# Kernel optimization log

Hardware: AMD Instinct MI355X
Metric: run time of the kernel (lower is better)

The kernel has to match this reference:

```python
import jax, jax.numpy as jnp
import numpy as np

DIM = 512
HEADS = 8
DIM_HEAD = 64
INNER = HEADS * DIM_HEAD  # 512
EPS = 1e-5
SCALE = DIM_HEAD ** (-0.5)


def setup_inputs() -> dict:
    key = jax.random.key(0)
    ks = jax.random.split(key, 12)
    B, S = 8, 1024
    x = jax.random.normal(ks[0], (B, DIM, S, 1), dtype=jnp.float32)
    # BatchNorm2d params (eval mode: running stats)
    bn_gamma = jax.random.normal(ks[1], (DIM,), dtype=jnp.float32) * 0.1 + 1.0
    bn_beta = jax.random.normal(ks[2], (DIM,), dtype=jnp.float32) * 0.1
    bn_mean = jax.random.normal(ks[3], (DIM,), dtype=jnp.float32) * 0.1
    bn_var = jax.random.uniform(ks[4], (DIM,), dtype=jnp.float32, minval=0.5, maxval=1.5)
    # 1x1 Conv2d == linear: weight [out, in], bias [out]
    def lin(k, out_d, in_d):
        kw, kb = jax.random.split(k)
        lim = 1.0 / np.sqrt(in_d)
        w = jax.random.uniform(kw, (out_d, in_d), dtype=jnp.float32, minval=-lim, maxval=lim)
        b = jax.random.uniform(kb, (out_d,), dtype=jnp.float32, minval=-lim, maxval=lim)
        return w, b
    wq, bq = lin(ks[5], INNER, DIM)
    wk, bk = lin(ks[6], INNER, DIM)
    wv, bv = lin(ks[7], INNER, DIM)
    wo, bo = lin(ks[8], DIM, INNER)
    return {"x": x, "bn_gamma": bn_gamma, "bn_beta": bn_beta,
            "bn_mean": bn_mean, "bn_var": bn_var,
            "wq": wq, "bq": bq, "wk": wk, "bk": bk,
            "wv": wv, "bv": bv, "wo": wo, "bo": bo}


def reference(x, bn_gamma, bn_beta, bn_mean, bn_var,
              wq, bq, wk, bk, wv, bv, wo, bo):
    B, C, S, _ = x.shape
    # BatchNorm2d (eval) over channel dim
    inv = jax.lax.rsqrt(bn_var + EPS)
    xn = (x - bn_mean[None, :, None, None]) * (bn_gamma * inv)[None, :, None, None] \
         + bn_beta[None, :, None, None]
    t = jnp.transpose(xn[..., 0], (0, 2, 1))  # [B, S, C]
    q = (t @ wq.T + bq).reshape(B, S, HEADS, DIM_HEAD)
    k = (t @ wk.T + bk).reshape(B, S, HEADS, DIM_HEAD)
    v = (t @ wv.T + bv).reshape(B, S, HEADS, DIM_HEAD)
    scores = jnp.einsum('bshd,bthd->bhst', q, k) * SCALE  # [B,H,S,S]
    attn = jax.nn.softmax(scores, axis=-1)
    o = jnp.einsum('bhst,bthd->bshd', attn, v).reshape(B, S, INNER)
    y = o @ wo.T + bo  # [B, S, C]
    return jnp.transpose(y, (0, 2, 1))[..., None]  # [B, C, S, 1]
```

## Files before the change

kernel.cpp:

```cpp
#include <hip/hip_runtime.h>
#include <stdint.h>

typedef __bf16 bf16;
typedef bf16 bf16x8 __attribute__((ext_vector_type(8)));
typedef bf16 bf16x4 __attribute__((ext_vector_type(4)));
typedef float f32x4 __attribute__((ext_vector_type(4)));

#define NB 8
#define NS 1024
#define NC 512
#define NH 8
#define ND 64

#define QSCALE 0.18033688011f

__device__ __forceinline__ void gload16(const void* g, void* l) {
  __builtin_amdgcn_global_load_lds(
      (const __attribute__((address_space(1))) void*)g,
      (__attribute__((address_space(3))) void*)l, 16, 0, 0);
}

__global__ __launch_bounds__(256) void bn_tr_kernel(
    const float* __restrict__ x, const float* __restrict__ gam,
    const float* __restrict__ bet, const float* __restrict__ mu,
    const float* __restrict__ var, bf16* __restrict__ t) {
  __shared__ float tile[32][33];
  const int b = blockIdx.z, c0 = blockIdx.y * 32, s0 = blockIdx.x * 32;
  const int tx = threadIdx.x, sj = tx & 31, ci = tx >> 5;
#pragma unroll
  for (int kk = 0; kk < 4; ++kk) {
    const int c = c0 + ci + (kk << 3);
    const float sc = gam[c] * rsqrtf(var[c] + 1e-5f);
    const float sh = bet[c] - mu[c] * sc;
    tile[ci + (kk << 3)][sj] = x[(size_t)(b * NC + c) * NS + s0 + sj] * sc + sh;
  }
  __syncthreads();
#pragma unroll
  for (int kk = 0; kk < 4; ++kk) {
    const int s = s0 + ci + (kk << 3);
    t[(size_t)(b * NS + s) * NC + c0 + sj] = (bf16)tile[sj][ci + (kk << 3)];
  }
}

__global__ __launch_bounds__(256) void wconv_kernel(
    const float* __restrict__ wq, const float* __restrict__ wk,
    const float* __restrict__ wv, const float* __restrict__ wo,
    bf16* __restrict__ wqb, bf16* __restrict__ wkb, bf16* __restrict__ wvb,
    bf16* __restrict__ wob) {
  const int i = (blockIdx.x * 256 + threadIdx.x) * 4;
  float4 a = *(const float4*)(&wq[i]);
  float4 b = *(const float4*)(&wk[i]);
  float4 c = *(const float4*)(&wv[i]);
  float4 d = *(const float4*)(&wo[i]);
  bf16x4 av = {(bf16)a.x, (bf16)a.y, (bf16)a.z, (bf16)a.w};
  bf16x4 bv = {(bf16)b.x, (bf16)b.y, (bf16)b.z, (bf16)b.w};
  bf16x4 cv = {(bf16)c.x, (bf16)c.y, (bf16)c.z, (bf16)c.w};
  bf16x4 dv = {(bf16)d.x, (bf16)d.y, (bf16)d.z, (bf16)d.w};
  *(bf16x4*)(&wqb[i]) = av;
  *(bf16x4*)(&wkb[i]) = bv;
  *(bf16x4*)(&wvb[i]) = cv;
  *(bf16x4*)(&wob[i]) = dv;
}

__global__ __launch_bounds__(256) void gemm_qkv_kernel(
    const bf16* __restrict__ t, const bf16* __restrict__ wqb,
    const bf16* __restrict__ wkb, const bf16* __restrict__ wvb,
    const float* __restrict__ bq, const float* __restrict__ bk,
    const float* __restrict__ bv, bf16* __restrict__ qo, bf16* __restrict__ ko,
    bf16* __restrict__ vo) {
  __shared__ __align__(16) bf16 As[128 * 32];
  __shared__ __align__(16) bf16 Bs[128 * 32];
  const int tid = threadIdx.x;
  const int m0 = blockIdx.x * 128, n0 = blockIdx.y * 128;
  const int wsel = n0 >> 9;
  const bf16* W = (wsel == 0) ? wqb : (wsel == 1 ? wkb : wvb);
  const float* bias = (wsel == 0) ? bq : (wsel == 1 ? bk : bv);
  const int nb = n0 & 511;
  const int w = tid >> 6, lane = tid & 63, l15 = lane & 15, l4 = lane >> 4;
  const int wm = (w >> 1) << 6, wn = (w & 1) << 6;

  const int srl = lane >> 2, sp = lane & 3;
  const int r0 = w * 16 + srl, r1 = 64 + w * 16 + srl;
  const int c0off = (sp ^ ((r0 >> 1) & 3)) << 3;
  const int c1off = (sp ^ ((r1 >> 1) & 3)) << 3;
  const bf16* a0 = t + (size_t)(m0 + r0) * 512 + c0off;
  const bf16* a1 = t + (size_t)(m0 + r1) * 512 + c1off;
  const bf16* b0 = W + (size_t)(nb + r0) * 512 + c0off;
  const bf16* b1 = W + (size_t)(nb + r1) * 512 + c1off;

  f32x4 acc[4][4] = {};
  for (int k0 = 0; k0 < 512; k0 += 32) {
    __syncthreads();
    gload16(a0 + k0, &As[w * 512]);
    gload16(a1 + k0, &As[2048 + w * 512]);
    gload16(b0 + k0, &Bs[w * 512]);
    gload16(b1 + k0, &Bs[2048 + w * 512]);
    __syncthreads();
    bf16x8 af[4], bfv[4];
#pragma unroll
    for (int mi = 0; mi < 4; ++mi) {
      const int row = wm + mi * 16 + l15;
      af[mi] = *(const bf16x8*)(&As[row * 32 + ((l4 ^ ((row >> 1) & 3)) << 3)]);
    }
#pragma unroll
    for (int ni = 0; ni < 4; ++ni) {
      const int row = wn + ni * 16 + l15;
      bfv[ni] = *(const bf16x8*)(&Bs[row * 32 + ((l4 ^ ((row >> 1) & 3)) << 3)]);
    }
#pragma unroll
    for (int mi = 0; mi < 4; ++mi)
#pragma unroll
      for (int ni = 0; ni < 4; ++ni)
        acc[mi][ni] = __builtin_amdgcn_mfma_f32_16x16x32_bf16(af[mi], bfv[ni],
                                                              acc[mi][ni], 0, 0, 0);
  }
  const int bidx = m0 >> 10;
  const int sbase = (m0 & 1023) + wm + (l4 << 2);
  if (wsel == 2) {
#pragma unroll
    for (int ni = 0; ni < 4; ++ni) {
      const int nn = nb + wn + ni * 16 + l15;
      const int hh = nn >> 6, dd = nn & 63;
      const float bsv = bias[nn];
      bf16* vbase = vo + (size_t)(bidx * NH + hh) * (ND * NS) + (size_t)dd * NS + sbase;
#pragma unroll
      for (int mi = 0; mi < 4; ++mi) {
        bf16x4 pk;
#pragma unroll
        for (int r = 0; r < 4; ++r) pk[r] = (bf16)(acc[mi][ni][r] + bsv);
        *(bf16x4*)(&vbase[mi * 16]) = pk;
      }
    }
  } else {
    const bool isq = (wsel == 0);
    bf16* outp = isq ? qo : ko;
#pragma unroll
    for (int ni = 0; ni < 4; ++ni) {
      const int nn = nb + wn + ni * 16 + l15;
      const int hh = nn >> 6, dd = nn & 63;
      const float bsv = bias[nn];
      bf16* obase = outp + (size_t)(bidx * NH + hh) * (NS * ND) + dd;
#pragma unroll
      for (int mi = 0; mi < 4; ++mi) {
#pragma unroll
        for (int r = 0; r < 4; ++r) {
          float val = acc[mi][ni][r] + bsv;
          if (isq) val *= QSCALE;
          obase[(size_t)(sbase + mi * 16 + r) * ND] = (bf16)val;
        }
      }
    }
  }
}

__global__ __launch_bounds__(512) void attn_kernel(const bf16* __restrict__ qg,
                                                   const bf16* __restrict__ kg,
                                                   const bf16* __restrict__ vtg,
                                                   bf16* __restrict__ og) {
  __shared__ __align__(16) bf16 Kb[2][64 * 64];
  __shared__ __align__(16) bf16 Vb[2][64 * 64];
  __shared__ __align__(16) bf16 Ps[8][16 * 64];
  const int bh = blockIdx.y, q0 = blockIdx.x * 128;
  const int tid = threadIdx.x, w = tid >> 6, lane = tid & 63;
  const int l15 = lane & 15, l4 = lane >> 4;
  const bf16* Qp = qg + ((size_t)bh * NS + q0) * ND;
  const bf16* Kp = kg + (size_t)bh * NS * ND;
  const bf16* Vp = vtg + (size_t)bh * ND * NS;

  bf16x8 qf[2];
#pragma unroll
  for (int kk = 0; kk < 2; ++kk)
    qf[kk] = *(const bf16x8*)(&Qp[(size_t)(w * 16 + l15) * ND + ((kk << 2) + l4) * 8]);

  const int srow = w * 8 + (lane >> 3);
  const int soff = ((lane & 7) ^ (srow & 7)) << 3;
  const bf16* ksrc = Kp + (size_t)srow * ND + soff;
  const bf16* vsrc = Vp + (size_t)srow * NS + soff;

  int foff[4][2];
#pragma unroll
  for (int rt = 0; rt < 4; ++rt) {
    const int row = rt * 16 + l15;
    foff[rt][0] = row * 64 + ((l4 ^ (row & 7)) << 3);
    foff[rt][1] = row * 64 + (((4 + l4) ^ (row & 7)) << 3);
  }

  f32x4 oacc[4] = {};
  float mrun = -1e30f, lrun = 0.f;

  gload16(ksrc, &Kb[0][w * 512]);
  gload16(vsrc, &Vb[0][w * 512]);
  __syncthreads();

  int buf = 0;
  for (int kv0 = 0; kv0 < NS; kv0 += 64, buf ^= 1) {
    if (kv0 + 64 < NS) {
      gload16(ksrc + (size_t)(kv0 + 64) * ND, &Kb[buf ^ 1][w * 512]);
      gload16(vsrc + (kv0 + 64), &Vb[buf ^ 1][w * 512]);
    }
    const bf16* Ks = Kb[buf];
    const bf16* Vs = Vb[buf];
    f32x4 st[4];
#pragma unroll
    for (int rt = 0; rt < 4; ++rt) {
      const bf16x8 a0 = *(const bf16x8*)(&Ks[foff[rt][0]]);
      const bf16x8 a1 = *(const bf16x8*)(&Ks[foff[rt][1]]);
      f32x4 z = {0.f, 0.f, 0.f, 0.f};
      z = __builtin_amdgcn_mfma_f32_16x16x32_bf16(a0, qf[0], z, 0, 0, 0);
      st[rt] = __builtin_amdgcn_mfma_f32_16x16x32_bf16(a1, qf[1], z, 0, 0, 0);
    }
    float pm = -1e30f;
#pragma unroll
    for (int rt = 0; rt < 4; ++rt)
#pragma unroll
      for (int r = 0; r < 4; ++r) pm = fmaxf(pm, st[rt][r]);
    pm = fmaxf(pm, __shfl_xor(pm, 16));
    pm = fmaxf(pm, __shfl_xor(pm, 32));
    if (!__all(pm - mrun <= 8.f)) {
      const float mnew = fmaxf(mrun, pm);
      const float alpha = __builtin_amdgcn_exp2f(mrun - mnew);
      float av[4];
#pragma unroll
      for (int r = 0; r < 4; ++r) av[r] = __shfl(alpha, (l4 << 2) + r);
#pragma unroll
      for (int di = 0; di < 4; ++di)
#pragma unroll
        for (int r = 0; r < 4; ++r) oacc[di][r] *= av[r];
      lrun *= alpha;
      mrun = mnew;
    }
    float rs = 0.f;
#pragma unroll
    for (int rt = 0; rt < 4; ++rt) {
      bf16x4 pk;
#pragma unroll
      for (int r = 0; r < 4; ++r) {
        const float p = __builtin_amdgcn_exp2f(st[rt][r] - mrun);
        rs += p;
        pk[r] = (bf16)p;
      }
      const int slot = (rt << 1) + (l4 >> 1);
      *(bf16x4*)(&Ps[w][l15 * 64 + ((slot ^ (l15 & 7)) << 3) + ((l4 & 1) << 2)]) = pk;
    }
    rs += __shfl_xor(rs, 16);
    rs += __shfl_xor(rs, 32);
    lrun += rs;
    bf16x8 pa[2];
#pragma unroll
    for (int kk = 0; kk < 2; ++kk)
      pa[kk] = *(const bf16x8*)(&Ps[w][l15 * 64 +
                                       ((((kk << 2) + l4) ^ (l15 & 7)) << 3)]);
#pragma unroll
    for (int di = 0; di < 4; ++di) {
      const bf16x8 v0 = *(const bf16x8*)(&Vs[foff[di][0]]);
      const bf16x8 v1 = *(const bf16x8*)(&Vs[foff[di][1]]);
      oacc[di] = __builtin_amdgcn_mfma_f32_16x16x32_bf16(pa[0], v0, oacc[di], 0, 0, 0);
      oacc[di] = __builtin_amdgcn_mfma_f32_16x16x32_bf16(pa[1], v1, oacc[di], 0, 0, 0);
    }
    __syncthreads();
  }
  float linv[4];
#pragma unroll
  for (int r = 0; r < 4; ++r) linv[r] = 1.f / __shfl(lrun, (l4 << 2) + r);
  const int b = bh >> 3, h = bh & 7;
  bf16* Op = og + (size_t)(b * NS + q0 + w * 16) * NC + h * ND;
#pragma unroll
  for (int di = 0; di < 4; ++di)
#pragma unroll
    for (int r = 0; r < 4; ++r)
      Op[(size_t)((l4 << 2) + r) * NC + di * 16 + l15] =
          (bf16)(oacc[di][r] * linv[r]);
}

__global__ __launch_bounds__(256) void gemm_out_kernel(
    const bf16* __restrict__ wob, const bf16* __restrict__ o,
    const float* __restrict__ bo, float* __restrict__ out) {
  __shared__ __align__(16) bf16 As[128 * 32];
  __shared__ __align__(16) bf16 Bs[128 * 32];
  const int tid = threadIdx.x;
  const int m0 = blockIdx.x * 128, n0 = blockIdx.y * 128;
  const int w = tid >> 6, lane = tid & 63, l15 = lane & 15, l4 = lane >> 4;
  const int wm = (w >> 1) << 6, wn = (w & 1) << 6;

  const int srl = lane >> 2, sp = lane & 3;
  const int r0 = w * 16 + srl, r1 = 64 + w * 16 + srl;
  const int c0off = (sp ^ ((r0 >> 1) & 3)) << 3;
  const int c1off = (sp ^ ((r1 >> 1) & 3)) << 3;
  const bf16* a0 = wob + (size_t)(m0 + r0) * 512 + c0off;
  const bf16* a1 = wob + (size_t)(m0 + r1) * 512 + c1off;
  const bf16* b0 = o + (size_t)(n0 + r0) * 512 + c0off;
  const bf16* b1 = o + (size_t)(n0 + r1) * 512 + c1off;

  f32x4 acc[4][4] = {};
  for (int k0 = 0; k0 < 512; k0 += 32) {
    __syncthreads();
    gload16(a0 + k0, &As[w * 512]);
    gload16(a1 + k0, &As[2048 + w * 512]);
    gload16(b0 + k0, &Bs[w * 512]);
    gload16(b1 + k0, &Bs[2048 + w * 512]);
    __syncthreads();
    bf16x8 af[4], bfv[4];
#pragma unroll
    for (int mi = 0; mi < 4; ++mi) {
      const int row = wm + mi * 16 + l15;
      af[mi] = *(const bf16x8*)(&As[row * 32 + ((l4 ^ ((row >> 1) & 3)) << 3)]);
    }
#pragma unroll
    for (int ni = 0; ni < 4; ++ni) {
      const int row = wn + ni * 16 + l15;
      bfv[ni] = *(const bf16x8*)(&Bs[row * 32 + ((l4 ^ ((row >> 1) & 3)) << 3)]);
    }
#pragma unroll
    for (int mi = 0; mi < 4; ++mi)
#pragma unroll
      for (int ni = 0; ni < 4; ++ni)
        acc[mi][ni] = __builtin_amdgcn_mfma_f32_16x16x32_bf16(af[mi], bfv[ni],
                                                              acc[mi][ni], 0, 0, 0);
  }
  const int b = n0 >> 10;
  const int sb = (n0 & 1023) + wn;
#pragma unroll
  for (int mi = 0; mi < 4; ++mi) {
#pragma unroll
    for (int r = 0; r < 4; ++r) {
      const int cout = m0 + wm + mi * 16 + (l4 << 2) + r;
      const float bsv = bo[cout];
#pragma unroll
      for (int ni = 0; ni < 4; ++ni)
        out[(size_t)(b * NC + cout) * NS + sb + ni * 16 + l15] =
            acc[mi][ni][r] + bsv;
    }
  }
}

extern "C" void kernel_launch(void* const* d_in, const int* in_sizes, int n_in,
                              void* d_out, int out_size, void* d_ws,
                              size_t ws_size, hipStream_t stream) {
  const float* x = (const float*)d_in[0];
  const float* gam = (const float*)d_in[1];
  const float* bet = (const float*)d_in[2];
  const float* mu = (const float*)d_in[3];
  const float* var = (const float*)d_in[4];
  const float* wq = (const float*)d_in[5];
  const float* bq = (const float*)d_in[6];
  const float* wk = (const float*)d_in[7];
  const float* bk = (const float*)d_in[8];
  const float* wv = (const float*)d_in[9];
  const float* bv = (const float*)d_in[10];
  const float* wo = (const float*)d_in[11];
  const float* bo = (const float*)d_in[12];
  float* out = (float*)d_out;

  char* p = (char*)d_ws;
  const size_t big = (size_t)8192 * 512 * sizeof(bf16);
  bf16* t = (bf16*)p;   p += big;
  bf16* q = (bf16*)p;   p += big;
  bf16* k = (bf16*)p;   p += big;
  bf16* vt = (bf16*)p;  p += big;
  const size_t wsz = (size_t)512 * 512 * sizeof(bf16);
  bf16* wqb = (bf16*)p; p += wsz;
  bf16* wkb = (bf16*)p; p += wsz;
  bf16* wvb = (bf16*)p; p += wsz;
  bf16* wob = (bf16*)p; p += wsz;
  bf16* o = t;

  bn_tr_kernel<<<dim3(32, 16, 8), 256, 0, stream>>>(x, gam, bet, mu, var, t);
  wconv_kernel<<<dim3(256), 256, 0, stream>>>(wq, wk, wv, wo, wqb, wkb, wvb, wob);
  gemm_qkv_kernel<<<dim3(64, 12), 256, 0, stream>>>(t, wqb, wkb, wvb, bq, bk, bv,
                                                    q, k, vt);
  attn_kernel<<<dim3(8, 64), 512, 0, stream>>>(q, k, vt, o);
  gemm_out_kernel<<<dim3(4, 64), 256, 0, stream>>>(wob, o, bo, out);
}
```

Before: 85.70 us.

## Double-buffer GEMM tiles, widen attention KV tile, vectorize transposed-fragment stores

Both projection GEMMs gain double-buffered LDS tiles so the next K slice loads while the current one is multiplied, removing one barrier per iteration. MFMA operand order is swapped for Q/K and the output GEMM so each lane holds contiguous outputs, allowing packed bf16x4 and float4 stores instead of scalar strided writes. The attention kernel processes 128 keys per iteration with doubled LDS buffers, transposes the P·V product so row scaling needs no cross-lane shuffles, adds setprio hints around MFMA bursts, and writes output with vector stores. The larger LDS footprint and occupancy hint may limit concurrency.

```diff
diff --git a/kernel.cpp b/kernel.cpp
--- a/kernel.cpp
+++ b/kernel.cpp
@@ -68,8 +68,8 @@
     const float* __restrict__ bq, const float* __restrict__ bk,
     const float* __restrict__ bv, bf16* __restrict__ qo, bf16* __restrict__ ko,
     bf16* __restrict__ vo) {
-  __shared__ __align__(16) bf16 As[128 * 32];
-  __shared__ __align__(16) bf16 Bs[128 * 32];
+  __shared__ __align__(16) bf16 As[2][128 * 32];
+  __shared__ __align__(16) bf16 Bs[2][128 * 32];
   const int tid = threadIdx.x;
   const int m0 = blockIdx.x * 128, n0 = blockIdx.y * 128;
   const int wsel = n0 >> 9;
@@ -89,34 +89,50 @@
   const bf16* b1 = W + (size_t)(nb + r1) * 512 + c1off;
 
   f32x4 acc[4][4] = {};
-  for (int k0 = 0; k0 < 512; k0 += 32) {
-    __syncthreads();
-    gload16(a0 + k0, &As[w * 512]);
-    gload16(a1 + k0, &As[2048 + w * 512]);
-    gload16(b0 + k0, &Bs[w * 512]);
-    gload16(b1 + k0, &Bs[2048 + w * 512]);
-    __syncthreads();
+  gload16(a0, &As[0][w * 512]);
+  gload16(a1, &As[0][2048 + w * 512]);
+  gload16(b0, &Bs[0][w * 512]);
+  gload16(b1, &Bs[0][2048 + w * 512]);
+  __syncthreads();
+  int buf = 0;
+  for (int k0 = 0; k0 < 512; k0 += 32, buf ^= 1) {
+    if (k0 + 32 < 512) {
+      gload16(a0 + k0 + 32, &As[buf ^ 1][w * 512]);
+      gload16(a1 + k0 + 32, &As[buf ^ 1][2048 + w * 512]);
+      gload16(b0 + k0 + 32, &Bs[buf ^ 1][w * 512]);
+      gload16(b1 + k0 + 32, &Bs[buf ^ 1][2048 + w * 512]);
+    }
     bf16x8 af[4], bfv[4];
 #pragma unroll
     for (int mi = 0; mi < 4; ++mi) {
       const int row = wm + mi * 16 + l15;
-      af[mi] = *(const bf16x8*)(&As[row * 32 + ((l4 ^ ((row >> 1) & 3)) << 3)]);
+      af[mi] = *(const bf16x8*)(&As[buf][row * 32 + ((l4 ^ ((row >> 1) & 3)) << 3)]);
     }
 #pragma unroll
     for (int ni = 0; ni < 4; ++ni) {
       const int row = wn + ni * 16 + l15;
-      bfv[ni] = *(const bf16x8*)(&Bs[row * 32 + ((l4 ^ ((row >> 1) & 3)) << 3)]);
-    }
-#pragma unroll
-    for (int mi = 0; mi < 4; ++mi)
-#pragma unroll
-      for (int ni = 0; ni < 4; ++ni)
-        acc[mi][ni] = __builtin_amdgcn_mfma_f32_16x16x32_bf16(af[mi], bfv[ni],
-                                                              acc[mi][ni], 0, 0, 0);
+      bfv[ni] = *(const bf16x8*)(&Bs[buf][row * 32 + ((l4 ^ ((row >> 1) & 3)) << 3)]);
+    }
+    if (wsel == 2) {
+#pragma unroll
+      for (int mi = 0; mi < 4; ++mi)
+#pragma unroll
+        for (int ni = 0; ni < 4; ++ni)
+          acc[mi][ni] = __builtin_amdgcn_mfma_f32_16x16x32_bf16(
+              af[mi], bfv[ni], acc[mi][ni], 0, 0, 0);
+    } else {
+#pragma unroll
+      for (int mi = 0; mi < 4; ++mi)
+#pragma unroll
+        for (int ni = 0; ni < 4; ++ni)
+          acc[mi][ni] = __builtin_amdgcn_mfma_f32_16x16x32_bf16(
+              bfv[ni], af[mi], acc[mi][ni], 0, 0, 0);
+    }
+    __syncthreads();
   }
   const int bidx = m0 >> 10;
-  const int sbase = (m0 & 1023) + wm + (l4 << 2);
   if (wsel == 2) {
+    const int sbase = (m0 & 1023) + wm + (l4 << 2);
 #pragma unroll
     for (int ni = 0; ni < 4; ++ni) {
       const int nn = nb + wn + ni * 16 + l15;
@@ -134,35 +150,38 @@
   } else {
     const bool isq = (wsel == 0);
     bf16* outp = isq ? qo : ko;
+    const int sbase = (m0 & 1023) + wm + l15;
 #pragma unroll
     for (int ni = 0; ni < 4; ++ni) {
-      const int nn = nb + wn + ni * 16 + l15;
-      const int hh = nn >> 6, dd = nn & 63;
-      const float bsv = bias[nn];
-      bf16* obase = outp + (size_t)(bidx * NH + hh) * (NS * ND) + dd;
+      const int nn0 = nb + wn + ni * 16 + (l4 << 2);
+      const int hh = nn0 >> 6, dd0 = nn0 & 63;
+      const float4 bs4 = *(const float4*)(&bias[nn0]);
+      bf16* obase = outp + (size_t)(bidx * NH + hh) * (NS * ND) + dd0;
 #pragma unroll
       for (int mi = 0; mi < 4; ++mi) {
+        bf16x4 pk;
+        const float* bp = (const float*)&bs4;
 #pragma unroll
         for (int r = 0; r < 4; ++r) {
-          float val = acc[mi][ni][r] + bsv;
+          float val = acc[mi][ni][r] + bp[r];
           if (isq) val *= QSCALE;
-          obase[(size_t)(sbase + mi * 16 + r) * ND] = (bf16)val;
+          pk[r] = (bf16)val;
         }
+        *(bf16x4*)(&obase[(size_t)(sbase + mi * 16) * ND]) = pk;
       }
     }
   }
 }
 
-__global__ __launch_bounds__(512) void attn_kernel(const bf16* __restrict__ qg,
-                                                   const bf16* __restrict__ kg,
-                                                   const bf16* __restrict__ vtg,
-                                                   bf16* __restrict__ og) {
-  __shared__ __align__(16) bf16 Kb[2][64 * 64];
-  __shared__ __align__(16) bf16 Vb[2][64 * 64];
+__global__ __launch_bounds__(512, 4) void attn_kernel(
+    const bf16* __restrict__ qg, const bf16* __restrict__ kg,
+    const bf16* __restrict__ vtg, bf16* __restrict__ og) {
+  __shared__ __align__(16) bf16 Kb[2][128 * 64];
+  __shared__ __align__(16) bf16 Vb[2][64 * 128];
   __shared__ __align__(16) bf16 Ps[8][16 * 64];
   const int bh = blockIdx.y, q0 = blockIdx.x * 128;
   const int tid = threadIdx.x, w = tid >> 6, lane = tid & 63;
-  const int l15 = lane & 15, l4 = lane >> 4;
+  const int l15 = lane & 15, l4 = lane >> 4, l7 = l15 & 7;
   const bf16* Qp = qg + ((size_t)bh * NS + q0) * ND;
   const bf16* Kp = kg + (size_t)bh * NS * ND;
   const bf16* Vp = vtg + (size_t)bh * ND * NS;
@@ -172,46 +191,48 @@
   for (int kk = 0; kk < 2; ++kk)
     qf[kk] = *(const bf16x8*)(&Qp[(size_t)(w * 16 + l15) * ND + ((kk << 2) + l4) * 8]);
 
-  const int srow = w * 8 + (lane >> 3);
-  const int soff = ((lane & 7) ^ (srow & 7)) << 3;
-  const bf16* ksrc = Kp + (size_t)srow * ND + soff;
-  const bf16* vsrc = Vp + (size_t)srow * NS + soff;
-
-  int foff[4][2];
-#pragma unroll
-  for (int rt = 0; rt < 4; ++rt) {
-    const int row = rt * 16 + l15;
-    foff[rt][0] = row * 64 + ((l4 ^ (row & 7)) << 3);
-    foff[rt][1] = row * 64 + (((4 + l4) ^ (row & 7)) << 3);
-  }
+  const int krow = w * 8 + (lane >> 3);
+  const int kcol = ((lane & 7) ^ (krow & 7)) << 3;
+  const bf16* ksrc = Kp + (size_t)krow * ND + kcol;
+  const int vrow = w * 4 + (lane >> 4);
+  const int vcol = ((lane & 15) ^ (vrow & 7)) << 3;
+  const bf16* vsrc = Vp + (size_t)vrow * NS + vcol;
 
   f32x4 oacc[4] = {};
   float mrun = -1e30f, lrun = 0.f;
 
   gload16(ksrc, &Kb[0][w * 512]);
+  gload16(ksrc + (size_t)64 * ND, &Kb[0][4096 + w * 512]);
   gload16(vsrc, &Vb[0][w * 512]);
+  gload16(vsrc + (size_t)32 * NS, &Vb[0][4096 + w * 512]);
   __syncthreads();
 
+  const int kb0 = l15 * 64 + ((l4 ^ l7) << 3);
+  const int kb1 = l15 * 64 + (((4 + l4) ^ l7) << 3);
   int buf = 0;
-  for (int kv0 = 0; kv0 < NS; kv0 += 64, buf ^= 1) {
-    if (kv0 + 64 < NS) {
-      gload16(ksrc + (size_t)(kv0 + 64) * ND, &Kb[buf ^ 1][w * 512]);
-      gload16(vsrc + (kv0 + 64), &Vb[buf ^ 1][w * 512]);
+  for (int kv0 = 0; kv0 < NS; kv0 += 128, buf ^= 1) {
+    if (kv0 + 128 < NS) {
+      gload16(ksrc + (size_t)(kv0 + 128) * ND, &Kb[buf ^ 1][w * 512]);
+      gload16(ksrc + (size_t)(kv0 + 192) * ND, &Kb[buf ^ 1][4096 + w * 512]);
+      gload16(vsrc + (kv0 + 128), &Vb[buf ^ 1][w * 512]);
+      gload16(vsrc + (size_t)32 * NS + (kv0 + 128), &Vb[buf ^ 1][4096 + w * 512]);
     }
     const bf16* Ks = Kb[buf];
     const bf16* Vs = Vb[buf];
-    f32x4 st[4];
-#pragma unroll
-    for (int rt = 0; rt < 4; ++rt) {
-      const bf16x8 a0 = *(const bf16x8*)(&Ks[foff[rt][0]]);
-      const bf16x8 a1 = *(const bf16x8*)(&Ks[foff[rt][1]]);
+    f32x4 st[8];
+    __builtin_amdgcn_s_setprio(1);
+#pragma unroll
+    for (int rt = 0; rt < 8; ++rt) {
+      const bf16x8 a0 = *(const bf16x8*)(&Ks[rt * 1024 + kb0]);
+      const bf16x8 a1 = *(const bf16x8*)(&Ks[rt * 1024 + kb1]);
       f32x4 z = {0.f, 0.f, 0.f, 0.f};
       z = __builtin_amdgcn_mfma_f32_16x16x32_bf16(a0, qf[0], z, 0, 0, 0);
       st[rt] = __builtin_amdgcn_mfma_f32_16x16x32_bf16(a1, qf[1], z, 0, 0, 0);
     }
+    __builtin_amdgcn_s_setprio(0);
     float pm = -1e30f;
 #pragma unroll
-    for (int rt = 0; rt < 4; ++rt)
+    for (int rt = 0; rt < 8; ++rt)
 #pragma unroll
       for (int r = 0; r < 4; ++r) pm = fmaxf(pm, st[rt][r]);
     pm = fmaxf(pm, __shfl_xor(pm, 16));
@@ -219,64 +240,66 @@
     if (!__all(pm - mrun <= 8.f)) {
       const float mnew = fmaxf(mrun, pm);
       const float alpha = __builtin_amdgcn_exp2f(mrun - mnew);
-      float av[4];
-#pragma unroll
-      for (int r = 0; r < 4; ++r) av[r] = __shfl(alpha, (l4 << 2) + r);
 #pragma unroll
       for (int di = 0; di < 4; ++di)
 #pragma unroll
-        for (int r = 0; r < 4; ++r) oacc[di][r] *= av[r];
+        for (int r = 0; r < 4; ++r) oacc[di][r] *= alpha;
       lrun *= alpha;
       mrun = mnew;
     }
     float rs = 0.f;
 #pragma unroll
-    for (int rt = 0; rt < 4; ++rt) {
-      bf16x4 pk;
-#pragma unroll
-      for (int r = 0; r < 4; ++r) {
-        const float p = __builtin_amdgcn_exp2f(st[rt][r] - mrun);
-        rs += p;
-        pk[r] = (bf16)p;
+    for (int h = 0; h < 2; ++h) {
+#pragma unroll
+      for (int rt4 = 0; rt4 < 4; ++rt4) {
+        const int rt = h * 4 + rt4;
+        bf16x4 pk;
+#pragma unroll
+        for (int r = 0; r < 4; ++r) {
+          const float p = __builtin_amdgcn_exp2f(st[rt][r] - mrun);
+          rs += p;
+          pk[r] = (bf16)p;
+        }
+        const int slot = (rt4 << 1) + (l4 >> 1);
+        *(bf16x4*)(&Ps[w][l15 * 64 + ((slot ^ l7) << 3) + ((l4 & 1) << 2)]) = pk;
       }
-      const int slot = (rt << 1) + (l4 >> 1);
-      *(bf16x4*)(&Ps[w][l15 * 64 + ((slot ^ (l15 & 7)) << 3) + ((l4 & 1) << 2)]) = pk;
-    }
-    rs += __shfl_xor(rs, 16);
-    rs += __shfl_xor(rs, 32);
+      bf16x8 pa0 = *(const bf16x8*)(&Ps[w][l15 * 64 + ((l4 ^ l7) << 3)]);
+      bf16x8 pa1 = *(const bf16x8*)(&Ps[w][l15 * 64 + (((4 + l4) ^ l7) << 3)]);
+      __builtin_amdgcn_s_setprio(1);
+#pragma unroll
+      for (int di = 0; di < 4; ++di) {
+        const int vb = (di * 16 + l15) * 128;
+        const bf16x8 v0 =
+            *(const bf16x8*)(&Vs[vb + ((((h << 3) + l4) ^ l7) << 3)]);
+        const bf16x8 v1 =
+            *(const bf16x8*)(&Vs[vb + ((((h << 3) + 4 + l4) ^ l7) << 3)]);
+        oacc[di] = __builtin_amdgcn_mfma_f32_16x16x32_bf16(v0, pa0, oacc[di], 0, 0, 0);
+        oacc[di] = __builtin_amdgcn_mfma_f32_16x16x32_bf16(v1, pa1, oacc[di], 0, 0, 0);
+      }
+      __builtin_amdgcn_s_setprio(0);
+    }
     lrun += rs;
-    bf16x8 pa[2];
-#pragma unroll
-    for (int kk = 0; kk < 2; ++kk)
-      pa[kk] = *(const bf16x8*)(&Ps[w][l15 * 64 +
-                                       ((((kk << 2) + l4) ^ (l15 & 7)) << 3)]);
-#pragma unroll
-    for (int di = 0; di < 4; ++di) {
-      const bf16x8 v0 = *(const bf16x8*)(&Vs[foff[di][0]]);
-      const bf16x8 v1 = *(const bf16x8*)(&Vs[foff[di][1]]);
-      oacc[di] = __builtin_amdgcn_mfma_f32_16x16x32_bf16(pa[0], v0, oacc[di], 0, 0, 0);
-      oacc[di] = __builtin_amdgcn_mfma_f32_16x16x32_bf16(pa[1], v1, oacc[di], 0, 0, 0);
-    }
     __syncthreads();
   }
-  float linv[4];
-#pragma unroll
-  for (int r = 0; r < 4; ++r) linv[r] = 1.f / __shfl(lrun, (l4 << 2) + r);
+  lrun += __shfl_xor(lrun, 16);
+  lrun += __shfl_xor(lrun, 32);
+  const float linv = 1.f / lrun;
   const int b = bh >> 3, h = bh & 7;
-  bf16* Op = og + (size_t)(b * NS + q0 + w * 16) * NC + h * ND;
-#pragma unroll
-  for (int di = 0; di < 4; ++di)
-#pragma unroll
-    for (int r = 0; r < 4; ++r)
-      Op[(size_t)((l4 << 2) + r) * NC + di * 16 + l15] =
-          (bf16)(oacc[di][r] * linv[r]);
+  bf16* Op = og + (size_t)(b * NS + q0 + w * 16 + l15) * NC + h * ND + (l4 << 2);
+#pragma unroll
+  for (int di = 0; di < 4; ++di) {
+    bf16x4 pk;
+#pragma unroll
+    for (int r = 0; r < 4; ++r) pk[r] = (bf16)(oacc[di][r] * linv);
+    *(bf16x4*)(&Op[di * 16]) = pk;
+  }
 }
 
 __global__ __launch_bounds__(256) void gemm_out_kernel(
     const bf16* __restrict__ wob, const bf16* __restrict__ o,
     const float* __restrict__ bo, float* __restrict__ out) {
-  __shared__ __align__(16) bf16 As[128 * 32];
-  __shared__ __align__(16) bf16 Bs[128 * 32];
+  __shared__ __align__(16) bf16 As[2][128 * 32];
+  __shared__ __align__(16) bf16 Bs[2][128 * 32];
   const int tid = threadIdx.x;
   const int m0 = blockIdx.x * 128, n0 = blockIdx.y * 128;
   const int w = tid >> 6, lane = tid & 63, l15 = lane & 15, l4 = lane >> 4;
@@ -292,43 +315,51 @@
   const bf16* b1 = o + (size_t)(n0 + r1) * 512 + c1off;
 
   f32x4 acc[4][4] = {};
-  for (int k0 = 0; k0 < 512; k0 += 32) {
-    __syncthreads();
-    gload16(a0 + k0, &As[w * 512]);
-    gload16(a1 + k0, &As[2048 + w * 512]);
-    gload16(b0 + k0, &Bs[w * 512]);
-    gload16(b1 + k0, &Bs[2048 + w * 512]);
-    __syncthreads();
+  gload16(a0, &As[0][w * 512]);
+  gload16(a1, &As[0][2048 + w * 512]);
+  gload16(b0, &Bs[0][w * 512]);
+  gload16(b1, &Bs[0][2048 + w * 512]);
+  __syncthreads();
+  int buf = 0;
+  for (int k0 = 0; k0 < 512; k0 += 32, buf ^= 1) {
+    if (k0 + 32 < 512) {
+      gload16(a0 + k0 + 32, &As[buf ^ 1][w * 512]);
+      gload16(a1 + k0 + 32, &As[buf ^ 1][2048 + w * 512]);
+      gload16(b0 + k0 + 32, &Bs[buf ^ 1][w * 512]);
+      gload16(b1 + k0 + 32, &Bs[buf ^ 1][2048 + w * 512]);
+    }
     bf16x8 af[4], bfv[4];
 #pragma unroll
     for (int mi = 0; mi < 4; ++mi) {
       const int row = wm + mi * 16 + l15;
-      af[mi] = *(const bf16x8*)(&As[row * 32 + ((l4 ^ ((row >> 1) & 3)) << 3)]);
+      af[mi] = *(const bf16x8*)(&As[buf][row * 32 + ((l4 ^ ((row >> 1) & 3)) << 3)]);
     }
 #pragma unroll
     for (int ni = 0; ni < 4; ++ni) {
       const int row = wn + ni * 16 + l15;
-      bfv[ni] = *(const bf16x8*)(&Bs[row * 32 + ((l4 ^ ((row >> 1) & 3)) << 3)]);
+      bfv[ni] = *(const bf16x8*)(&Bs[buf][row * 32 + ((l4 ^ ((row >> 1) & 3)) << 3)]);
     }
 #pragma unroll
     for (int mi = 0; mi < 4; ++mi)
 #pragma unroll
       for (int ni = 0; ni < 4; ++ni)
-        acc[mi][ni] = __builtin_amdgcn_mfma_f32_16x16x32_bf16(af[mi], bfv[ni],
-                                                              acc[mi][ni], 0, 0, 0);
+        acc[mi][ni] = __builtin_amdgcn_mfma_f32_16x16x32_bf16(
+            bfv[ni], af[mi], acc[mi][ni], 0, 0, 0);
+    __syncthreads();
   }
   const int b = n0 >> 10;
   const int sb = (n0 & 1023) + wn;
 #pragma unroll
   for (int mi = 0; mi < 4; ++mi) {
-#pragma unroll
-    for (int r = 0; r < 4; ++r) {
-      const int cout = m0 + wm + mi * 16 + (l4 << 2) + r;
-      const float bsv = bo[cout];
-#pragma unroll
-      for (int ni = 0; ni < 4; ++ni)
-        out[(size_t)(b * NC + cout) * NS + sb + ni * 16 + l15] =
-            acc[mi][ni][r] + bsv;
+    const int cout = m0 + wm + mi * 16 + l15;
+    const float bsv = bo[cout];
+    float* obase = out + (size_t)(b * NC + cout) * NS;
+#pragma unroll
+    for (int ni = 0; ni < 4; ++ni) {
+      const int s0i = sb + ni * 16 + (l4 << 2);
+      float4 pk = {acc[mi][ni][0] + bsv, acc[mi][ni][1] + bsv,
+                   acc[mi][ni][2] + bsv, acc[mi][ni][3] + bsv};
+      *(float4*)(&obase[s0i]) = pk;
     }
   }
 }
```

Measured after the change: 93.09 us. 1.09x slower.
